# Kernel tuning notes

Measured on AMD Instinct MI355X. Metric: run time of the kernel, lower is better.

The kernel has to match this reference:

```python
import jax, jax.numpy as jnp
import numpy as np

B = 4096       # batch of instance features
N = 131072     # num_samples (cluster memory slots)
D = 256        # num_features
TEMP = 0.05
EPS = 1e-12    # F.normalize eps


def setup_inputs() -> dict:
    key = jax.random.key(0)
    k1, k2, k3 = jax.random.split(key, 3)
    inputs = jax.random.normal(k1, (B, D), dtype=jnp.float32)
    targets = jax.random.randint(k2, (B,), 0, N, dtype=jnp.int64)
    # learned/buffer memory bank; original registers zeros but is populated with
    # L2-normalized cluster centroids before use -> initialize likewise
    feats = jax.random.normal(k3, (N, D), dtype=jnp.float32)
    feats = feats / jnp.linalg.norm(feats, axis=1, keepdims=True)
    feature_memory = jnp.zeros((1,), dtype=jnp.float32)  # unused by forward
    return {"inputs": inputs, "targets": targets, "feature_memory": feature_memory,
            "k": 10, "features": feats}


def reference(inputs, targets, feature_memory, k, features):
    # inputs: [B, D], targets: [B] int, features: [N, D]
    # F.normalize(inputs, dim=1)
    nrm = jnp.linalg.norm(inputs, axis=1, keepdims=True)
    x = inputs / jnp.maximum(nrm, EPS)
    # CM_Hard forward output: x @ features.T  (the per-cluster argmin loop has
    # no effect on the forward output; it only drives the buffer EMA in backward)
    logits = jnp.matmul(x, features.T) / TEMP          # [B, N]
    # F.cross_entropy(logits, targets), mean reduction
    lse = jax.nn.logsumexp(logits, axis=1)             # [B]
    tgt_logit = jnp.take_along_axis(logits, targets[:, None].astype(jnp.int32), axis=1)[:, 0]
    loss = jnp.mean(lse - tgt_logit)
    return loss
```

## Files before the change

kernel.cpp:

```cpp
#include <hip/hip_runtime.h>
#include <hip/hip_bf16.h>


typedef __attribute__((ext_vector_type(8))) short bf16x8;
typedef __attribute__((ext_vector_type(4))) float f32x4;
typedef __attribute__((address_space(1))) unsigned int u32g;
typedef __attribute__((address_space(3))) unsigned int u32l;

#define B_ROWS   4096
#define N_FEATS  131072
#define D_DIM    256
#define SCALE_B2 28.853900817779268f
#define LN2F     0.69314718055994531f

#define BM 128
#define BN 128
#define BKT 64
#define NCHUNK 16
#define COLS_PB (N_FEATS / NCHUNK)
#define NTILES  (COLS_PB / BN)
#define TILE_B  (BN * BKT * 2)
#define NSLICE  (NCHUNK * 2)

#define E2(x) __builtin_amdgcn_exp2f(x)

static __device__ __forceinline__ unsigned short f2bf(float x) {
    __hip_bfloat16 h = __float2bfloat16(x);
    return __builtin_bit_cast(unsigned short, h);
}
static __device__ __forceinline__ float bf2f(unsigned short u) {
    return __builtin_bit_cast(float, ((unsigned int)u) << 16);
}

__global__ __launch_bounds__(64) void k_normalize(const float* __restrict__ in,
                                                  unsigned short* __restrict__ xb) {
    const int row  = blockIdx.x;
    const int lane = threadIdx.x;
    float4 v = *(const float4*)(in + (size_t)row * D_DIM + lane * 4);
    float ss = v.x * v.x + v.y * v.y + v.z * v.z + v.w * v.w;
#pragma unroll
    for (int mask = 1; mask < 64; mask <<= 1) ss += __shfl_xor(ss, mask);
    const float sc = SCALE_B2 / fmaxf(sqrtf(ss), 1e-12f);
    ushort4 o;
    o.x = f2bf(v.x * sc); o.y = f2bf(v.y * sc);
    o.z = f2bf(v.z * sc); o.w = f2bf(v.w * sc);
    *(ushort4*)(xb + (size_t)row * D_DIM + lane * 4) = o;
}

__global__ __launch_bounds__(256) void k_cvt_feats(const float* __restrict__ f,
                                                   unsigned short* __restrict__ fb) {
    const int total4 = N_FEATS * D_DIM / 4;
    const int stride = gridDim.x * blockDim.x;
    for (int i = blockIdx.x * blockDim.x + threadIdx.x; i < total4; i += stride) {
        float4 v = ((const float4*)f)[i];
        ushort4 o;
        o.x = f2bf(v.x); o.y = f2bf(v.y); o.z = f2bf(v.z); o.w = f2bf(v.w);
        ((ushort4*)fb)[i] = o;
    }
}

#define STAGE(t_, bOff_) do {                                                         \
        const int nt_ = (t_) >> 2, kt_ = (t_) & 3;                                    \
        const unsigned short* s_ = fb + (nbase + (size_t)nt_ * BN) * D_DIM + kt_ * BKT; \
        char* d_ = &Bs[(bOff_) + dBase];                                              \
        __builtin_amdgcn_global_load_lds((const u32g*)(s_ + e0), (u32l*)d_, 16, 0, 0);\
        __builtin_amdgcn_global_load_lds((const u32g*)(s_ + e1), (u32l*)(d_ + 8192), 16, 0, 0); \
    } while (0)

#define COMPUTE(ktL, bOff_) do {                                                      \
        const char* buf_ = &Bs[(bOff_)];                                              \
        bf16x8 bfr[2][4];                                                             \
        _Pragma("unroll")                                                             \
        for (int ks2 = 0; ks2 < 2; ++ks2)                                             \
        _Pragma("unroll")                                                             \
            for (int n = 0; n < 4; ++n)                                               \
                bfr[ks2][n] = *(const bf16x8*)(buf_ + dsOff[ks2][n]);                 \
        __builtin_amdgcn_s_setprio(1);                                                \
        _Pragma("unroll")                                                             \
        for (int ks2 = 0; ks2 < 2; ++ks2)                                             \
        _Pragma("unroll")                                                             \
            for (int m = 0; m < 2; ++m)                                               \
        _Pragma("unroll")                                                             \
                for (int n = 0; n < 4; ++n)                                           \
                    acc[m][n] = __builtin_amdgcn_mfma_f32_16x16x32_bf16(              \
                        afr[m][(ktL) * 2 + ks2], bfr[ks2][n], acc[m][n], 0, 0, 0);    \
        __builtin_amdgcn_s_setprio(0);                                                \
    } while (0)

#define WC(n_)  asm volatile("s_waitcnt vmcnt(" #n_ ")" ::: "memory")
#define VMB(n_) asm volatile("s_waitcnt vmcnt(" #n_ ")\ns_barrier" ::: "memory")

#define EPI() do {                                                                    \
        _Pragma("unroll")                                                             \
        for (int m = 0; m < 2; ++m)                                                   \
        _Pragma("unroll")                                                             \
            for (int j = 0; j < 4; ++j) {                                             \
                const int r = m * 4 + j;                                              \
                s_run[r] += (E2(acc[m][0][j]) + E2(acc[m][1][j]))                     \
                          + (E2(acc[m][2][j]) + E2(acc[m][3][j]));                    \
            }                                                                         \
        _Pragma("unroll")                                                             \
        for (int m = 0; m < 2; ++m)                                                   \
        _Pragma("unroll")                                                             \
            for (int n = 0; n < 4; ++n) acc[m][n] = (f32x4){0.f, 0.f, 0.f, 0.f};      \
    } while (0)

#define LOADCVT(t_) do {                                                              \
        const int nt_ = (t_) >> 2, kt_ = (t_) & 3;                                    \
        const float* s0_ = featf + (nbase + (size_t)nt_ * BN + fc0) * D_DIM + kt_ * BKT + fk0; \
        const float* s1_ = featf + (nbase + (size_t)nt_ * BN + fc1) * D_DIM + kt_ * BKT + fk1; \
        float4 a0 = *(const float4*)s0_, a1 = *(const float4*)(s0_ + 4);              \
        float4 b0 = *(const float4*)s1_, b1 = *(const float4*)(s1_ + 4);              \
        unsigned short ua[8] = {f2bf(a0.x), f2bf(a0.y), f2bf(a0.z), f2bf(a0.w),       \
                                f2bf(a1.x), f2bf(a1.y), f2bf(a1.z), f2bf(a1.w)};      \
        unsigned short ub[8] = {f2bf(b0.x), f2bf(b0.y), f2bf(b0.z), f2bf(b0.w),       \
                                f2bf(b1.x), f2bf(b1.y), f2bf(b1.z), f2bf(b1.w)};      \
        ra = *(int4*)ua; rb = *(int4*)ub;                                             \
    } while (0)
#define WRITEB(bOff_) do {                                                            \
        char* d_ = &Bs[(bOff_)];                                                      \
        *(int4*)(d_ + wo0) = ra;                                                      \
        *(int4*)(d_ + wo1) = rb;                                                      \
    } while (0)

template <bool BF16B>
__global__ __launch_bounds__(512, 2) void k_lse_gemm(
    const unsigned short* __restrict__ xb,
    const float* __restrict__ featf,
    const unsigned short* __restrict__ fb,
    float* __restrict__ partials)
{
    __shared__ char Bs[4 * TILE_B];

    const int hw  = blockIdx.y * 32 + blockIdx.x;
    const int lid = (hw & 7) * 64 + (hw >> 3);
    const int bx  = lid & 31;
    const int by  = lid >> 5;

    const int tid  = threadIdx.x;
    const int lane = tid & 63;
    const int w    = tid >> 6;
    const int wr   = w >> 1;
    const int wc   = w & 1;
    const int l15  = lane & 15;
    const int l4   = lane >> 4;

    const int brow     = bx * BM;
    const size_t nbase = (size_t)by * COLS_PB;

    int dsOff[2][4];
#pragma unroll
    for (int ks2 = 0; ks2 < 2; ++ks2)
#pragma unroll
        for (int n = 0; n < 4; ++n) {
            const int col = wc * 64 + n * 16 + l15;
            dsOff[ks2][n] = (col * 128 + ks2 * 64 + l4 * 16) ^ ((col & 7) << 4);
        }

    bf16x8 afr[2][8];
#pragma unroll
    for (int m = 0; m < 2; ++m) {
        const unsigned short* ap =
            xb + (size_t)(brow + wr * 32 + m * 16 + l15) * D_DIM + l4 * 8;
#pragma unroll
        for (int ks = 0; ks < 8; ++ks)
            afr[m][ks] = *(const bf16x8*)(ap + ks * 32);
    }

    f32x4 acc[2][4];
#pragma unroll
    for (int m = 0; m < 2; ++m)
#pragma unroll
        for (int n = 0; n < 4; ++n) acc[m][n] = (f32x4){0.f, 0.f, 0.f, 0.f};
    float s_run[8];
#pragma unroll
    for (int r = 0; r < 8; ++r) s_run[r] = 0.f;

    if (BF16B) {
        int e0, e1;
        {
            const int p0 = w * 1024 + lane * 16;
            const int c0 = p0 >> 7;
            e0 = c0 * D_DIM + ((((p0 ^ ((c0 & 7) << 4)) >> 4) & 7) * 8);
            const int p1 = p0 + 8192;
            const int c1 = p1 >> 7;
            e1 = c1 * D_DIM + ((((p1 ^ ((c1 & 7) << 4)) >> 4) & 7) * 8);
        }
        const int dBase = w * 1024;

        STAGE(0, 0);
        STAGE(1, TILE_B);
        for (int nt = 0; nt < NTILES - 1; ++nt) {
            const int t0 = nt * 4;
            VMB(2);
            STAGE(t0 + 2, 2 * TILE_B);
            COMPUTE(0, 0);
            WC(2);
            STAGE(t0 + 3, 3 * TILE_B);
            COMPUTE(1, TILE_B);
            VMB(2);
            STAGE(t0 + 4, 0);
            COMPUTE(2, 2 * TILE_B);
            WC(2);
            STAGE(t0 + 5, TILE_B);
            COMPUTE(3, 3 * TILE_B);
            EPI();
        }
        {
            const int t0 = (NTILES - 1) * 4;
            VMB(2);
            STAGE(t0 + 2, 2 * TILE_B);
            COMPUTE(0, 0);
            WC(2);
            STAGE(t0 + 3, 3 * TILE_B);
            COMPUTE(1, TILE_B);
            VMB(2);
            COMPUTE(2, 2 * TILE_B);
            WC(0);
            COMPUTE(3, 3 * TILE_B);
            EPI();
        }
    } else {
        const int c0 = tid, c1 = tid + 512;
        const int fc0 = c0 >> 3, fk0 = (c0 & 7) * 8;
        const int fc1 = c1 >> 3, fk1 = (c1 & 7) * 8;
        const int wo0 = (fc0 * 128 + fk0 * 2) ^ ((fc0 & 7) << 4);
        const int wo1 = (fc1 * 128 + fk1 * 2) ^ ((fc1 & 7) << 4);
        int4 ra, rb;
        LOADCVT(0); WRITEB(0);
        __syncthreads();
        for (int nt = 0; nt < NTILES; ++nt) {
            { LOADCVT(nt * 4 + 1); COMPUTE(0, 0); WRITEB(TILE_B); __syncthreads(); }
            { LOADCVT(nt * 4 + 2); COMPUTE(1, TILE_B); WRITEB(0); __syncthreads(); }
            { LOADCVT(nt * 4 + 3); COMPUTE(2, 0); WRITEB(TILE_B); __syncthreads(); }
            {
                if (nt < NTILES - 1) LOADCVT(nt * 4 + 4);
                COMPUTE(3, TILE_B);
                EPI();
                if (nt < NTILES - 1) { WRITEB(0); }
                __syncthreads();
            }
        }
    }

#pragma unroll
    for (int r = 0; r < 8; ++r) {
        float S = s_run[r];
#pragma unroll
        for (int mask = 1; mask < 16; mask <<= 1) S += __shfl_xor(S, mask);
        s_run[r] = S;
    }
    if (l15 == 0) {
        const int slice = by * 2 + wc;
#pragma unroll
        for (int r = 0; r < 8; ++r) {
            const int m = r >> 2, j = r & 3;
            const int row = brow + wr * 32 + m * 16 + l4 * 4 + j;
            partials[(size_t)row * NSLICE + slice] = s_run[r];
        }
    }
}

__global__ __launch_bounds__(64) void k_finalize(const float* __restrict__ partials,
                                                 const unsigned short* __restrict__ xb,
                                                 const float* __restrict__ feats,
                                                 const int* __restrict__ targets,
                                                 float* __restrict__ loss) {
    const int row  = blockIdx.x;
    const int lane = threadIdx.x;
    float S = (lane < NSLICE) ? partials[(size_t)row * NSLICE + lane] : 0.0f;

    const int t = targets[row];
    ushort4 xv = *(const ushort4*)(xb + (size_t)row * D_DIM + lane * 4);
    float4  fv = *(const float4*)(feats + (size_t)t * D_DIM + lane * 4);
    float dot = bf2f(xv.x) * fv.x + bf2f(xv.y) * fv.y +
                bf2f(xv.z) * fv.z + bf2f(xv.w) * fv.w;
#pragma unroll
    for (int mask = 1; mask < 64; mask <<= 1) {
        S   += __shfl_xor(S, mask);
        dot += __shfl_xor(dot, mask);
    }
    if (lane == 0) loss[row] = LN2F * (__builtin_amdgcn_logf(S) - dot);
}

__global__ __launch_bounds__(256) void k_reduce(const float* __restrict__ loss,
                                                float* __restrict__ out) {
    __shared__ float sm[4];
    const int tid = threadIdx.x;
    float s = 0.f;
    for (int i = tid; i < B_ROWS; i += 256) s += loss[i];
#pragma unroll
    for (int mask = 1; mask < 64; mask <<= 1) s += __shfl_xor(s, mask);
    if ((tid & 63) == 0) sm[tid >> 6] = s;
    __syncthreads();
    if (tid == 0) out[0] = (sm[0] + sm[1] + sm[2] + sm[3]) * (1.0f / B_ROWS);
}

extern "C" void kernel_launch(void* const* d_in, const int* in_sizes, int n_in,
                              void* d_out, int out_size, void* d_ws, size_t ws_size,
                              hipStream_t stream) {
    const float* inputs  = (const float*)d_in[0];
    const int*   targets = (const int*)d_in[1];
    const float* feats   = (const float*)d_in[4];
    float* out = (float*)d_out;

    char* ws = (char*)d_ws;
    const size_t off_xb       = 0;
    const size_t off_partials = off_xb + (size_t)B_ROWS * D_DIM * 2;
    const size_t off_loss     = off_partials + (size_t)B_ROWS * NSLICE * sizeof(float);
    const size_t off_fb       = off_loss + (size_t)B_ROWS * sizeof(float);
    const size_t need_fb      = off_fb + (size_t)N_FEATS * D_DIM * 2;

    unsigned short* xb = (unsigned short*)(ws + off_xb);
    float* partials    = (float*)(ws + off_partials);
    float* loss        = (float*)(ws + off_loss);
    unsigned short* fb = (unsigned short*)(ws + off_fb);
    const bool precvt  = ws_size >= need_fb;

    k_normalize<<<B_ROWS, 64, 0, stream>>>(inputs, xb);
    if (precvt) {
        k_cvt_feats<<<2048, 256, 0, stream>>>(feats, fb);
        k_lse_gemm<true><<<dim3(32, NCHUNK), 512, 0, stream>>>(xb, feats, fb, partials);
    } else {
        k_lse_gemm<false><<<dim3(32, NCHUNK), 512, 0, stream>>>(xb, feats, fb, partials);
    }
    k_finalize<<<B_ROWS, 64, 0, stream>>>(partials, xb, feats, targets, loss);
    k_reduce<<<1, 256, 0, stream>>>(loss, out);
}
```

Measured before the change: 279.5 us.

## Switch GEMM inner loop to 32x32x16 bf16 MFMA with new LDS fragment layout

Replaces the 16x16x32 MFMA tiling (2x4 accumulators per wave) with two 32x32x16 MFMA accumulators per wave. A-fragments, LDS read offsets with swizzle, the exp2 epilogue and the row-sum reduction/write-out are all remapped to the 32x32 output layout. The goal is fewer MFMA issues and fewer LDS reads per tile, since B fragments are loaded once per k-step per 32 columns. The epilogue now keeps 16 running sums per lane and a 32-lane shuffle reduction. The row-mapping and swizzle math must match the MFMA layout exactly or results are wrong.

```diff
diff --git a/kernel.cpp b/kernel.cpp
--- a/kernel.cpp
+++ b/kernel.cpp
@@ -3,7 +3,7 @@
 
 
 typedef __attribute__((ext_vector_type(8))) short bf16x8;
-typedef __attribute__((ext_vector_type(4))) float f32x4;
+typedef __attribute__((ext_vector_type(16))) float f32x16;
 typedef __attribute__((address_space(1))) unsigned int u32g;
 typedef __attribute__((address_space(3))) unsigned int u32l;
 
@@ -69,21 +69,16 @@
 
 #define COMPUTE(ktL, bOff_) do {                                                      \
         const char* buf_ = &Bs[(bOff_)];                                              \
-        bf16x8 bfr[2][4];                                                             \
-        _Pragma("unroll")                                                             \
-        for (int ks2 = 0; ks2 < 2; ++ks2)                                             \
-        _Pragma("unroll")                                                             \
-            for (int n = 0; n < 4; ++n)                                               \
-                bfr[ks2][n] = *(const bf16x8*)(buf_ + dsOff[ks2][n]);                 \
         __builtin_amdgcn_s_setprio(1);                                                \
         _Pragma("unroll")                                                             \
-        for (int ks2 = 0; ks2 < 2; ++ks2)                                             \
-        _Pragma("unroll")                                                             \
-            for (int m = 0; m < 2; ++m)                                               \
-        _Pragma("unroll")                                                             \
-                for (int n = 0; n < 4; ++n)                                           \
-                    acc[m][n] = __builtin_amdgcn_mfma_f32_16x16x32_bf16(              \
-                        afr[m][(ktL) * 2 + ks2], bfr[ks2][n], acc[m][n], 0, 0, 0);    \
+        for (int ks = 0; ks < 4; ++ks) {                                              \
+            bf16x8 b0 = *(const bf16x8*)(buf_ + (A0 ^ (ks << 5)));                    \
+            bf16x8 b1 = *(const bf16x8*)(buf_ + (A1 ^ (ks << 5)));                    \
+            acc0 = __builtin_amdgcn_mfma_f32_32x32x16_bf16(                           \
+                afr[(ktL) * 4 + ks], b0, acc0, 0, 0, 0);                              \
+            acc1 = __builtin_amdgcn_mfma_f32_32x32x16_bf16(                           \
+                afr[(ktL) * 4 + ks], b1, acc1, 0, 0, 0);                              \
+        }                                                                             \
         __builtin_amdgcn_s_setprio(0);                                                \
     } while (0)
 
@@ -92,17 +87,10 @@
 
 #define EPI() do {                                                                    \
         _Pragma("unroll")                                                             \
-        for (int m = 0; m < 2; ++m)                                                   \
-        _Pragma("unroll")                                                             \
-            for (int j = 0; j < 4; ++j) {                                             \
-                const int r = m * 4 + j;                                              \
-                s_run[r] += (E2(acc[m][0][j]) + E2(acc[m][1][j]))                     \
-                          + (E2(acc[m][2][j]) + E2(acc[m][3][j]));                    \
-            }                                                                         \
-        _Pragma("unroll")                                                             \
-        for (int m = 0; m < 2; ++m)                                                   \
-        _Pragma("unroll")                                                             \
-            for (int n = 0; n < 4; ++n) acc[m][n] = (f32x4){0.f, 0.f, 0.f, 0.f};      \
+        for (int rg = 0; rg < 16; ++rg) {                                             \
+            s_run[rg] += E2(acc0[rg]) + E2(acc1[rg]);                                 \
+            acc0[rg] = 0.f; acc1[rg] = 0.f;                                           \
+        }                                                                             \
     } while (0)
 
 #define LOADCVT(t_) do {                                                              \
@@ -142,39 +130,36 @@
     const int w    = tid >> 6;
     const int wr   = w >> 1;
     const int wc   = w & 1;
-    const int l15  = lane & 15;
-    const int l4   = lane >> 4;
+    const int l31  = lane & 31;
+    const int hl   = lane >> 5;
 
     const int brow     = bx * BM;
     const size_t nbase = (size_t)by * COLS_PB;
 
-    int dsOff[2][4];
-#pragma unroll
-    for (int ks2 = 0; ks2 < 2; ++ks2)
-#pragma unroll
-        for (int n = 0; n < 4; ++n) {
-            const int col = wc * 64 + n * 16 + l15;
-            dsOff[ks2][n] = (col * 128 + ks2 * 64 + l4 * 16) ^ ((col & 7) << 4);
-        }
-
-    bf16x8 afr[2][8];
-#pragma unroll
-    for (int m = 0; m < 2; ++m) {
+    int A0, A1;
+    {
+        const int b = lane & 7;
+        const int lowbits = ((hl ^ (b & 1)) << 4) + (((b >> 1) & 3) << 5);
+        const int col0 = wc * 64 + l31;
+        A0 = col0 * 128 + lowbits;
+        A1 = (col0 + 32) * 128 + lowbits;
+    }
+
+    bf16x8 afr[16];
+    {
         const unsigned short* ap =
-            xb + (size_t)(brow + wr * 32 + m * 16 + l15) * D_DIM + l4 * 8;
-#pragma unroll
-        for (int ks = 0; ks < 8; ++ks)
-            afr[m][ks] = *(const bf16x8*)(ap + ks * 32);
-    }
-
-    f32x4 acc[2][4];
-#pragma unroll
-    for (int m = 0; m < 2; ++m)
-#pragma unroll
-        for (int n = 0; n < 4; ++n) acc[m][n] = (f32x4){0.f, 0.f, 0.f, 0.f};
-    float s_run[8];
-#pragma unroll
-    for (int r = 0; r < 8; ++r) s_run[r] = 0.f;
+            xb + (size_t)(brow + wr * 32 + l31) * D_DIM + hl * 8;
+#pragma unroll
+        for (int ks = 0; ks < 16; ++ks)
+            afr[ks] = *(const bf16x8*)(ap + ks * 16);
+    }
+
+    f32x16 acc0, acc1;
+#pragma unroll
+    for (int rg = 0; rg < 16; ++rg) { acc0[rg] = 0.f; acc1[rg] = 0.f; }
+    float s_run[16];
+#pragma unroll
+    for (int rg = 0; rg < 16; ++rg) s_run[rg] = 0.f;
 
     if (BF16B) {
         int e0, e1;
@@ -244,19 +229,18 @@
     }
 
 #pragma unroll
-    for (int r = 0; r < 8; ++r) {
-        float S = s_run[r];
-#pragma unroll
-        for (int mask = 1; mask < 16; mask <<= 1) S += __shfl_xor(S, mask);
-        s_run[r] = S;
-    }
-    if (l15 == 0) {
+    for (int rg = 0; rg < 16; ++rg) {
+        float S = s_run[rg];
+#pragma unroll
+        for (int mask = 1; mask < 32; mask <<= 1) S += __shfl_xor(S, mask);
+        s_run[rg] = S;
+    }
+    if (l31 == 0) {
         const int slice = by * 2 + wc;
 #pragma unroll
-        for (int r = 0; r < 8; ++r) {
-            const int m = r >> 2, j = r & 3;
-            const int row = brow + wr * 32 + m * 16 + l4 * 4 + j;
-            partials[(size_t)row * NSLICE + slice] = s_run[r];
+        for (int rg = 0; rg < 16; ++rg) {
+            const int row = brow + wr * 32 + (rg & 3) + 8 * (rg >> 2) + 4 * hl;
+            partials[(size_t)row * NSLICE + slice] = s_run[rg];
         }
     }
 }
```

After: 296.7 us. 6.1% more time.

## Restage bf16 pipeline to two-tile pairs and fold accumulator zeroing into MFMA

Applied to the files above, without the earlier changes.

The main loop now waits once per pair of k-tiles (vmcnt 0 plus barrier) and issues two stages at a time, instead of alternating single-tile waits. The exp2 epilogue moves ahead of the next tile's compute so it can overlap outstanding loads. The explicit accumulator reset is replaced by passing a zero C operand to the first MFMA of each tile. This cuts barrier count and VALU zeroing, but the full vmcnt(0) waits may expose more memory latency.

```diff
diff --git a/kernel.cpp b/kernel.cpp
--- a/kernel.cpp
+++ b/kernel.cpp
@@ -67,7 +67,7 @@
         __builtin_amdgcn_global_load_lds((const u32g*)(s_ + e1), (u32l*)(d_ + 8192), 16, 0, 0); \
     } while (0)
 
-#define COMPUTE(ktL, bOff_) do {                                                      \
+#define COMPUTE(ktL, bOff_, ZC_) do {                                                 \
         const char* buf_ = &Bs[(bOff_)];                                              \
         bf16x8 bfr[2][4];                                                             \
         _Pragma("unroll")                                                             \
@@ -81,13 +81,15 @@
         _Pragma("unroll")                                                             \
             for (int m = 0; m < 2; ++m)                                               \
         _Pragma("unroll")                                                             \
-                for (int n = 0; n < 4; ++n)                                           \
+                for (int n = 0; n < 4; ++n) {                                         \
+                    const f32x4 cin_ = ((ZC_) && ks2 == 0) ? (f32x4){0.f, 0.f, 0.f, 0.f} \
+                                                           : acc[m][n];               \
                     acc[m][n] = __builtin_amdgcn_mfma_f32_16x16x32_bf16(              \
-                        afr[m][(ktL) * 2 + ks2], bfr[ks2][n], acc[m][n], 0, 0, 0);    \
+                        afr[m][(ktL) * 2 + ks2], bfr[ks2][n], cin_, 0, 0, 0);         \
+                }                                                                     \
         __builtin_amdgcn_s_setprio(0);                                                \
     } while (0)
 
-#define WC(n_)  asm volatile("s_waitcnt vmcnt(" #n_ ")" ::: "memory")
 #define VMB(n_) asm volatile("s_waitcnt vmcnt(" #n_ ")\ns_barrier" ::: "memory")
 
 #define EPI() do {                                                                    \
@@ -99,10 +101,6 @@
                 s_run[r] += (E2(acc[m][0][j]) + E2(acc[m][1][j]))                     \
                           + (E2(acc[m][2][j]) + E2(acc[m][3][j]));                    \
             }                                                                         \
-        _Pragma("unroll")                                                             \
-        for (int m = 0; m < 2; ++m)                                                   \
-        _Pragma("unroll")                                                             \
-            for (int n = 0; n < 4; ++n) acc[m][n] = (f32x4){0.f, 0.f, 0.f, 0.f};      \
     } while (0)
 
 #define LOADCVT(t_) do {                                                              \
@@ -190,34 +188,30 @@
 
         STAGE(0, 0);
         STAGE(1, TILE_B);
-        for (int nt = 0; nt < NTILES - 1; ++nt) {
+        VMB(0);
+        STAGE(2, 2 * TILE_B); STAGE(3, 3 * TILE_B);
+        COMPUTE(0, 0, true); COMPUTE(1, TILE_B, false);
+        VMB(0);
+        STAGE(4, 0); STAGE(5, TILE_B);
+        COMPUTE(2, 2 * TILE_B, false); COMPUTE(3, 3 * TILE_B, false);
+        for (int nt = 1; nt < NTILES - 1; ++nt) {
             const int t0 = nt * 4;
-            VMB(2);
-            STAGE(t0 + 2, 2 * TILE_B);
-            COMPUTE(0, 0);
-            WC(2);
-            STAGE(t0 + 3, 3 * TILE_B);
-            COMPUTE(1, TILE_B);
-            VMB(2);
-            STAGE(t0 + 4, 0);
-            COMPUTE(2, 2 * TILE_B);
-            WC(2);
-            STAGE(t0 + 5, TILE_B);
-            COMPUTE(3, 3 * TILE_B);
+            VMB(0);
+            STAGE(t0 + 2, 2 * TILE_B); STAGE(t0 + 3, 3 * TILE_B);
             EPI();
+            COMPUTE(0, 0, true); COMPUTE(1, TILE_B, false);
+            VMB(0);
+            STAGE(t0 + 4, 0); STAGE(t0 + 5, TILE_B);
+            COMPUTE(2, 2 * TILE_B, false); COMPUTE(3, 3 * TILE_B, false);
         }
         {
             const int t0 = (NTILES - 1) * 4;
-            VMB(2);
-            STAGE(t0 + 2, 2 * TILE_B);
-            COMPUTE(0, 0);
-            WC(2);
-            STAGE(t0 + 3, 3 * TILE_B);
-            COMPUTE(1, TILE_B);
-            VMB(2);
-            COMPUTE(2, 2 * TILE_B);
-            WC(0);
-            COMPUTE(3, 3 * TILE_B);
+            VMB(0);
+            STAGE(t0 + 2, 2 * TILE_B); STAGE(t0 + 3, 3 * TILE_B);
+            EPI();
+            COMPUTE(0, 0, true); COMPUTE(1, TILE_B, false);
+            VMB(0);
+            COMPUTE(2, 2 * TILE_B, false); COMPUTE(3, 3 * TILE_B, false);
             EPI();
         }
     } else {
@@ -230,12 +224,12 @@
         LOADCVT(0); WRITEB(0);
         __syncthreads();
         for (int nt = 0; nt < NTILES; ++nt) {
-            { LOADCVT(nt * 4 + 1); COMPUTE(0, 0); WRITEB(TILE_B); __syncthreads(); }
-            { LOADCVT(nt * 4 + 2); COMPUTE(1, TILE_B); WRITEB(0); __syncthreads(); }
-            { LOADCVT(nt * 4 + 3); COMPUTE(2, 0); WRITEB(TILE_B); __syncthreads(); }
+            { LOADCVT(nt * 4 + 1); COMPUTE(0, 0, true); WRITEB(TILE_B); __syncthreads(); }
+            { LOADCVT(nt * 4 + 2); COMPUTE(1, TILE_B, false); WRITEB(0); __syncthreads(); }
+            { LOADCVT(nt * 4 + 3); COMPUTE(2, 0, false); WRITEB(TILE_B); __syncthreads(); }
             {
                 if (nt < NTILES - 1) LOADCVT(nt * 4 + 4);
-                COMPUTE(3, TILE_B);
+                COMPUTE(3, TILE_B, false);
                 EPI();
                 if (nt < NTILES - 1) { WRITEB(0); }
                 __syncthreads();
```

Measured after the change: 280.6 us. Within noise of the previous version (+0.4%).
